# Kernel optimization log

Measured on AMD Instinct MI355X. Metric: run time of the kernel, lower is better.

The kernel has to match this reference:

```python
import jax, jax.numpy as jnp
import numpy as np

B, T, H = 16, 4096, 512


def setup_inputs() -> dict:
    key = jax.random.key(0)
    k1, k2, k3 = jax.random.split(key, 3)
    inputs = jax.random.normal(k1, (B, T, H), dtype=jnp.float32)
    # lengths in [1, T] so the global mean pool is well-defined
    lengths = jax.random.randint(k2, (B,), 1, T + 1, dtype=jnp.int32)
    mask = jax.random.randint(k3, (B, T), 0, 2).astype(bool)
    return {"inputs": inputs, "lengths": lengths, "mask": mask}


def _mean_pool(x, lengths):
    # length-masked mean pool: [B, T, H] -> [B, H]
    t = x.shape[1]
    valid = (jnp.arange(t)[None, :] < lengths[:, None]).astype(x.dtype)  # [B, T]
    summed = jnp.einsum('bth,bt->bh', x, valid)
    denom = jnp.maximum(lengths, 1).astype(x.dtype)[:, None]
    return summed / denom


def _span_select(x, mask):
    # Compact masked tokens to the front of each row (stable order), zero the tail.
    # Equivalent to the TF while_loop + scatter_nd/gather_nd compaction:
    # stable argsort of ~mask puts True positions first, in original order.
    order = jnp.argsort(jnp.logical_not(mask), axis=1, stable=True)  # [B, T]
    dense = jnp.take_along_axis(x, order[:, :, None], axis=1)        # [B, T, H]
    span_lengths = jnp.sum(mask.astype(jnp.int32), axis=1)           # [B]
    dense_mask = jnp.arange(x.shape[1])[None, :] < span_lengths[:, None]
    dense = dense * dense_mask[:, :, None].astype(x.dtype)
    return dense, span_lengths


def reference(inputs, lengths, mask):
    global_view = _mean_pool(inputs, lengths)            # [B, H]
    spans, span_lengths = _span_select(inputs, mask)     # [B, T, H], [B]
    local_view = _mean_pool(spans, span_lengths)         # [B, H]
    return jnp.concatenate([global_view, local_view], axis=-1)  # [B, 2H]
```

## Files before the change

### kernel.cpp

```cpp
#include <hip/hip_runtime.h>


constexpr int Bc = 16;
constexpr int Tc = 4096;
constexpr int Hc = 512;
constexpr int CHUNK  = 64;
constexpr int NCHUNK = Tc / CHUNK;
constexpr int NBLK   = Bc * NCHUNK;


__global__ __launch_bounds__(128) void glp_partial(
    const float* __restrict__ x,
    const int* __restrict__ lengths,
    const int* __restrict__ mask,
    float* __restrict__ pg,
    float* __restrict__ pl,
    int*   __restrict__ pcnt)
{
    const int blk  = blockIdx.x;
    const int b    = blk >> 6;
    const int c    = blk & (NCHUNK - 1);
    const int t0   = c * CHUNK;
    const int lane = threadIdx.x;
    const int len  = lengths[b];

    const float4* __restrict__ xb =
        (const float4*)x + ((size_t)b * Tc + t0) * (Hc / 4) + lane;
    const int* __restrict__ mb = mask + (size_t)b * Tc + t0;

    float4 g = make_float4(0.f, 0.f, 0.f, 0.f);
    float4 l = make_float4(0.f, 0.f, 0.f, 0.f);
    int mc = 0;

    for (int ii = 0; ii < CHUNK; ii += 8) {
        float4 v[8];
        int    m[8];
        #pragma unroll
        for (int j = 0; j < 8; ++j) {
            v[j] = xb[(size_t)(ii + j) * (Hc / 4)];
            m[j] = mb[ii + j];
        }
        #pragma unroll
        for (int j = 0; j < 8; ++j) {
            const float wg = (t0 + ii + j < len) ? 1.f : 0.f;
            const float wl = m[j] ? 1.f : 0.f;
            g.x = fmaf(v[j].x, wg, g.x); g.y = fmaf(v[j].y, wg, g.y);
            g.z = fmaf(v[j].z, wg, g.z); g.w = fmaf(v[j].w, wg, g.w);
            l.x = fmaf(v[j].x, wl, l.x); l.y = fmaf(v[j].y, wl, l.y);
            l.z = fmaf(v[j].z, wl, l.z); l.w = fmaf(v[j].w, wl, l.w);
            mc += (m[j] != 0);
        }
    }

    ((float4*)(pg + (size_t)blk * Hc))[lane] = g;
    ((float4*)(pl + (size_t)blk * Hc))[lane] = l;
    if (lane == 0) pcnt[blk] = mc;
}

__global__ __launch_bounds__(512) void glp_reduce(
    const float* __restrict__ pg,
    const float* __restrict__ pl,
    const int* __restrict__ pcnt,
    const int* __restrict__ lengths,
    float* __restrict__ out)
{
    const int b = blockIdx.x;
    const int h = threadIdx.x;
    const float* pgb = pg + (size_t)b * NCHUNK * Hc + h;
    const float* plb = pl + (size_t)b * NCHUNK * Hc + h;
    float gs = 0.f, ls = 0.f;
    #pragma unroll 8
    for (int c = 0; c < NCHUNK; ++c) {
        gs += pgb[(size_t)c * Hc];
        ls += plb[(size_t)c * Hc];
    }
    int cntv = 0;
    for (int c = 0; c < NCHUNK; ++c) cntv += pcnt[b * NCHUNK + c];
    out[b * 2 * Hc + h]      = gs / (float)max(lengths[b], 1);
    out[b * 2 * Hc + Hc + h] = ls / (float)max(cntv, 1);
}


__global__ __launch_bounds__(128) void glp_partial_atomic(
    const float* __restrict__ x,
    const int* __restrict__ lengths,
    const int* __restrict__ mask,
    float* __restrict__ gsum, float* __restrict__ lsum, int* __restrict__ cnt)
{
    const int blk  = blockIdx.x;
    const int b    = blk >> 6;
    const int c    = blk & (NCHUNK - 1);
    const int t0   = c * CHUNK;
    const int lane = threadIdx.x;
    const int len  = lengths[b];
    const float4* __restrict__ xb =
        (const float4*)x + ((size_t)b * Tc + t0) * (Hc / 4) + lane;
    const int* __restrict__ mb = mask + (size_t)b * Tc + t0;

    float4 g = make_float4(0.f, 0.f, 0.f, 0.f);
    float4 l = make_float4(0.f, 0.f, 0.f, 0.f);
    int mc = 0;
    for (int ii = 0; ii < CHUNK; ii += 8) {
        float4 v[8]; int m[8];
        #pragma unroll
        for (int j = 0; j < 8; ++j) { v[j] = xb[(size_t)(ii + j) * (Hc / 4)]; m[j] = mb[ii + j]; }
        #pragma unroll
        for (int j = 0; j < 8; ++j) {
            const float wg = (t0 + ii + j < len) ? 1.f : 0.f;
            const float wl = m[j] ? 1.f : 0.f;
            g.x = fmaf(v[j].x, wg, g.x); g.y = fmaf(v[j].y, wg, g.y);
            g.z = fmaf(v[j].z, wg, g.z); g.w = fmaf(v[j].w, wg, g.w);
            l.x = fmaf(v[j].x, wl, l.x); l.y = fmaf(v[j].y, wl, l.y);
            l.z = fmaf(v[j].z, wl, l.z); l.w = fmaf(v[j].w, wl, l.w);
            mc += (m[j] != 0);
        }
    }
    float* gp = gsum + b * Hc + lane * 4;
    float* lp = lsum + b * Hc + lane * 4;
    atomicAdd(gp + 0, g.x); atomicAdd(gp + 1, g.y);
    atomicAdd(gp + 2, g.z); atomicAdd(gp + 3, g.w);
    atomicAdd(lp + 0, l.x); atomicAdd(lp + 1, l.y);
    atomicAdd(lp + 2, l.z); atomicAdd(lp + 3, l.w);
    if (lane == 0) atomicAdd(cnt + b, mc);
}

__global__ __launch_bounds__(512) void glp_finalize(
    const float* __restrict__ gsum, const float* __restrict__ lsum,
    const int* __restrict__ cnt, const int* __restrict__ lengths,
    float* __restrict__ out)
{
    const int b = blockIdx.x;
    const int h = threadIdx.x;
    out[b * 2 * Hc + h]      = gsum[b * Hc + h] / (float)max(lengths[b], 1);
    out[b * 2 * Hc + Hc + h] = lsum[b * Hc + h] / (float)max(cnt[b], 1);
}

extern "C" void kernel_launch(void* const* d_in, const int* in_sizes, int n_in,
                              void* d_out, int out_size, void* d_ws, size_t ws_size,
                              hipStream_t stream) {
    const float* x     = (const float*)d_in[0];
    const int* lengths = (const int*)d_in[1];
    const int* mask    = (const int*)d_in[2];
    float* out = (float*)d_out;

    const size_t need = (size_t)NBLK * Hc * sizeof(float) * 2 + NBLK * sizeof(int);
    if (ws_size >= need) {
        float* pg  = (float*)d_ws;
        float* pl  = pg + (size_t)NBLK * Hc;
        int* pcnt  = (int*)(pl + (size_t)NBLK * Hc);
        glp_partial<<<NBLK, 128, 0, stream>>>(x, lengths, mask, pg, pl, pcnt);
        glp_reduce<<<Bc, Hc, 0, stream>>>(pg, pl, pcnt, lengths, out);
    } else {
        float* gsum = (float*)d_ws;
        float* lsum = gsum + Bc * Hc;
        int*   cnt  = (int*)(lsum + Bc * Hc);
        const size_t zb = (size_t)(2 * Bc * Hc) * sizeof(float) + Bc * sizeof(int);
        hipMemsetAsync(d_ws, 0, zb, stream);
        glp_partial_atomic<<<NBLK, 128, 0, stream>>>(x, lengths, mask, gsum, lsum, cnt);
        glp_finalize<<<Bc, Hc, 0, stream>>>(gsum, lsum, cnt, lengths, out);
    }
}
```

Baseline: 199.4 us.

## Split token chunks finer with two-way parallel rows and hierarchical reduce

Shrinks each partial-sum block to 16 tokens with 256 threads, two threads per column handling alternate tokens, and issues all loads up front. This raises the number of blocks and the loads in flight, to hide memory latency in the streaming pass. Because the partial buffer grows, a two-stage reduction replaces the single per-batch reduce. The cost is extra workspace traffic for the larger partial arrays.

```diff
diff --git a/kernel.cpp b/kernel.cpp
--- a/kernel.cpp
+++ b/kernel.cpp
@@ -4,12 +4,16 @@
 constexpr int Bc = 16;
 constexpr int Tc = 4096;
 constexpr int Hc = 512;
-constexpr int CHUNK  = 64;
-constexpr int NCHUNK = Tc / CHUNK;
-constexpr int NBLK   = Bc * NCHUNK;
-
-
-__global__ __launch_bounds__(128) void glp_partial(
+constexpr int H4 = Hc / 4;
+constexpr int CHUNK   = 16;
+constexpr int NCHUNK  = Tc / CHUNK;
+constexpr int NBLK    = Bc * NCHUNK;
+constexpr int NROW    = NBLK * 2;
+constexpr int ROWS_PB = NROW / Bc;
+constexpr int G2      = 8;
+constexpr int R2ROWS  = ROWS_PB / G2;
+
+__global__ __launch_bounds__(256) void glp_partial(
     const float* __restrict__ x,
     const int* __restrict__ lengths,
     const int* __restrict__ mask,
@@ -18,28 +22,128 @@
     int*   __restrict__ pcnt)
 {
     const int blk  = blockIdx.x;
-    const int b    = blk >> 6;
+    const int b    = blk >> 8;
     const int c    = blk & (NCHUNK - 1);
     const int t0   = c * CHUNK;
-    const int lane = threadIdx.x;
+    const int lane = threadIdx.x & 127;
+    const int par  = threadIdx.x >> 7;
     const int len  = lengths[b];
 
     const float4* __restrict__ xb =
-        (const float4*)x + ((size_t)b * Tc + t0) * (Hc / 4) + lane;
-    const int* __restrict__ mb = mask + (size_t)b * Tc + t0;
+        (const float4*)x + ((size_t)b * Tc + t0 + par) * H4 + lane;
+    const int* __restrict__ mb = mask + (size_t)b * Tc + t0 + par;
+
+    float4 v[8]; int m[8];
+    #pragma unroll
+    for (int j = 0; j < 8; ++j) {
+        v[j] = xb[(size_t)(2 * j) * H4];
+        m[j] = mb[2 * j];
+    }
 
     float4 g = make_float4(0.f, 0.f, 0.f, 0.f);
     float4 l = make_float4(0.f, 0.f, 0.f, 0.f);
     int mc = 0;
-
-    for (int ii = 0; ii < CHUNK; ii += 8) {
-        float4 v[8];
-        int    m[8];
+    #pragma unroll
+    for (int j = 0; j < 8; ++j) {
+        const float wg = (t0 + par + 2 * j < len) ? 1.f : 0.f;
+        const float wl = m[j] ? 1.f : 0.f;
+        g.x = fmaf(v[j].x, wg, g.x); g.y = fmaf(v[j].y, wg, g.y);
+        g.z = fmaf(v[j].z, wg, g.z); g.w = fmaf(v[j].w, wg, g.w);
+        l.x = fmaf(v[j].x, wl, l.x); l.y = fmaf(v[j].y, wl, l.y);
+        l.z = fmaf(v[j].z, wl, l.z); l.w = fmaf(v[j].w, wl, l.w);
+        mc += (m[j] != 0);
+    }
+
+    const int row = blk * 2 + par;
+    ((float4*)(pg + (size_t)row * Hc))[lane] = g;
+    ((float4*)(pl + (size_t)row * Hc))[lane] = l;
+    if (lane == 0) pcnt[row] = mc;
+}
+
+__global__ __launch_bounds__(128) void glp_reduce1(
+    const float* __restrict__ pg, const float* __restrict__ pl,
+    const int* __restrict__ pcnt,
+    float* __restrict__ qg, float* __restrict__ ql, int* __restrict__ qcnt)
+{
+    const int blk  = blockIdx.x;
+    const int r0   = blk * R2ROWS;
+    const int lane = threadIdx.x;
+    const float4* pg4 = (const float4*)pg + (size_t)r0 * H4 + lane;
+    const float4* pl4 = (const float4*)pl + (size_t)r0 * H4 + lane;
+
+    float4 gs = make_float4(0.f, 0.f, 0.f, 0.f);
+    float4 ls = make_float4(0.f, 0.f, 0.f, 0.f);
+    for (int r = 0; r < R2ROWS; r += 8) {
+        float4 a[8], d[8];
         #pragma unroll
         for (int j = 0; j < 8; ++j) {
-            v[j] = xb[(size_t)(ii + j) * (Hc / 4)];
-            m[j] = mb[ii + j];
+            a[j] = pg4[(size_t)(r + j) * H4];
+            d[j] = pl4[(size_t)(r + j) * H4];
         }
+        #pragma unroll
+        for (int j = 0; j < 8; ++j) {
+            gs.x += a[j].x; gs.y += a[j].y; gs.z += a[j].z; gs.w += a[j].w;
+            ls.x += d[j].x; ls.y += d[j].y; ls.z += d[j].z; ls.w += d[j].w;
+        }
+    }
+    ((float4*)(qg + (size_t)blk * Hc))[lane] = gs;
+    ((float4*)(ql + (size_t)blk * Hc))[lane] = ls;
+    if (lane == 0) {
+        int mc = 0;
+        for (int r = 0; r < R2ROWS; ++r) mc += pcnt[r0 + r];
+        qcnt[blk] = mc;
+    }
+}
+
+__global__ __launch_bounds__(128) void glp_reduce2(
+    const float* __restrict__ qg, const float* __restrict__ ql,
+    const int* __restrict__ qcnt, const int* __restrict__ lengths,
+    float* __restrict__ out)
+{
+    const int b    = blockIdx.x;
+    const int lane = threadIdx.x;
+    float4 gs = make_float4(0.f, 0.f, 0.f, 0.f);
+    float4 ls = make_float4(0.f, 0.f, 0.f, 0.f);
+    #pragma unroll
+    for (int k = 0; k < G2; ++k) {
+        float4 a = ((const float4*)(qg + (size_t)(b * G2 + k) * Hc))[lane];
+        float4 d = ((const float4*)(ql + (size_t)(b * G2 + k) * Hc))[lane];
+        gs.x += a.x; gs.y += a.y; gs.z += a.z; gs.w += a.w;
+        ls.x += d.x; ls.y += d.y; ls.z += d.z; ls.w += d.w;
+    }
+    int cnt = 0;
+    #pragma unroll
+    for (int k = 0; k < G2; ++k) cnt += qcnt[b * G2 + k];
+    const float invl = 1.f / (float)max(lengths[b], 1);
+    const float invc = 1.f / (float)max(cnt, 1);
+    gs.x *= invl; gs.y *= invl; gs.z *= invl; gs.w *= invl;
+    ls.x *= invc; ls.y *= invc; ls.z *= invc; ls.w *= invc;
+    ((float4*)(out + (size_t)b * 2 * Hc))[lane]      = gs;
+    ((float4*)(out + (size_t)b * 2 * Hc + Hc))[lane] = ls;
+}
+
+__global__ __launch_bounds__(128) void glp_partial_atomic(
+    const float* __restrict__ x, const int* __restrict__ lengths,
+    const int* __restrict__ mask,
+    float* __restrict__ gsum, float* __restrict__ lsum, int* __restrict__ cnt)
+{
+    const int blk  = blockIdx.x;
+    const int b    = blk >> 6;
+    const int c    = blk & 63;
+    const int t0   = c * 64;
+    const int lane = threadIdx.x;
+    const int len  = lengths[b];
+    const float4* __restrict__ xb =
+        (const float4*)x + ((size_t)b * Tc + t0) * H4 + lane;
+    const int* __restrict__ mb = mask + (size_t)b * Tc + t0;
+
+    float4 g = make_float4(0.f, 0.f, 0.f, 0.f);
+    float4 l = make_float4(0.f, 0.f, 0.f, 0.f);
+    int mc = 0;
+    for (int ii = 0; ii < 64; ii += 8) {
+        float4 v[8]; int m[8];
+        #pragma unroll
+        for (int j = 0; j < 8; ++j) { v[j] = xb[(size_t)(ii + j) * H4]; m[j] = mb[ii + j]; }
         #pragma unroll
         for (int j = 0; j < 8; ++j) {
             const float wg = (t0 + ii + j < len) ? 1.f : 0.f;
@@ -51,70 +155,6 @@
             mc += (m[j] != 0);
         }
     }
-
-    ((float4*)(pg + (size_t)blk * Hc))[lane] = g;
-    ((float4*)(pl + (size_t)blk * Hc))[lane] = l;
-    if (lane == 0) pcnt[blk] = mc;
-}
-
-__global__ __launch_bounds__(512) void glp_reduce(
-    const float* __restrict__ pg,
-    const float* __restrict__ pl,
-    const int* __restrict__ pcnt,
-    const int* __restrict__ lengths,
-    float* __restrict__ out)
-{
-    const int b = blockIdx.x;
-    const int h = threadIdx.x;
-    const float* pgb = pg + (size_t)b * NCHUNK * Hc + h;
-    const float* plb = pl + (size_t)b * NCHUNK * Hc + h;
-    float gs = 0.f, ls = 0.f;
-    #pragma unroll 8
-    for (int c = 0; c < NCHUNK; ++c) {
-        gs += pgb[(size_t)c * Hc];
-        ls += plb[(size_t)c * Hc];
-    }
-    int cntv = 0;
-    for (int c = 0; c < NCHUNK; ++c) cntv += pcnt[b * NCHUNK + c];
-    out[b * 2 * Hc + h]      = gs / (float)max(lengths[b], 1);
-    out[b * 2 * Hc + Hc + h] = ls / (float)max(cntv, 1);
-}
-
-
-__global__ __launch_bounds__(128) void glp_partial_atomic(
-    const float* __restrict__ x,
-    const int* __restrict__ lengths,
-    const int* __restrict__ mask,
-    float* __restrict__ gsum, float* __restrict__ lsum, int* __restrict__ cnt)
-{
-    const int blk  = blockIdx.x;
-    const int b    = blk >> 6;
-    const int c    = blk & (NCHUNK - 1);
-    const int t0   = c * CHUNK;
-    const int lane = threadIdx.x;
-    const int len  = lengths[b];
-    const float4* __restrict__ xb =
-        (const float4*)x + ((size_t)b * Tc + t0) * (Hc / 4) + lane;
-    const int* __restrict__ mb = mask + (size_t)b * Tc + t0;
-
-    float4 g = make_float4(0.f, 0.f, 0.f, 0.f);
-    float4 l = make_float4(0.f, 0.f, 0.f, 0.f);
-    int mc = 0;
-    for (int ii = 0; ii < CHUNK; ii += 8) {
-        float4 v[8]; int m[8];
-        #pragma unroll
-        for (int j = 0; j < 8; ++j) { v[j] = xb[(size_t)(ii + j) * (Hc / 4)]; m[j] = mb[ii + j]; }
-        #pragma unroll
-        for (int j = 0; j < 8; ++j) {
-            const float wg = (t0 + ii + j < len) ? 1.f : 0.f;
-            const float wl = m[j] ? 1.f : 0.f;
-            g.x = fmaf(v[j].x, wg, g.x); g.y = fmaf(v[j].y, wg, g.y);
-            g.z = fmaf(v[j].z, wg, g.z); g.w = fmaf(v[j].w, wg, g.w);
-            l.x = fmaf(v[j].x, wl, l.x); l.y = fmaf(v[j].y, wl, l.y);
-            l.z = fmaf(v[j].z, wl, l.z); l.w = fmaf(v[j].w, wl, l.w);
-            mc += (m[j] != 0);
-        }
-    }
     float* gp = gsum + b * Hc + lane * 4;
     float* lp = lsum + b * Hc + lane * 4;
     atomicAdd(gp + 0, g.x); atomicAdd(gp + 1, g.y);
@@ -143,20 +183,27 @@
     const int* mask    = (const int*)d_in[2];
     float* out = (float*)d_out;
 
-    const size_t need = (size_t)NBLK * Hc * sizeof(float) * 2 + NBLK * sizeof(int);
+    const size_t npg   = (size_t)NROW * Hc;
+    const size_t nq    = (size_t)Bc * G2 * Hc;
+    const size_t need  = (2 * npg + 2 * nq) * sizeof(float)
+                       + (NROW + Bc * G2) * sizeof(int);
     if (ws_size >= need) {
-        float* pg  = (float*)d_ws;
-        float* pl  = pg + (size_t)NBLK * Hc;
-        int* pcnt  = (int*)(pl + (size_t)NBLK * Hc);
-        glp_partial<<<NBLK, 128, 0, stream>>>(x, lengths, mask, pg, pl, pcnt);
-        glp_reduce<<<Bc, Hc, 0, stream>>>(pg, pl, pcnt, lengths, out);
+        float* pg   = (float*)d_ws;
+        float* pl   = pg + npg;
+        float* qg   = pl + npg;
+        float* ql   = qg + nq;
+        int*   pcnt = (int*)(ql + nq);
+        int*   qcnt = pcnt + NROW;
+        glp_partial<<<NBLK, 256, 0, stream>>>(x, lengths, mask, pg, pl, pcnt);
+        glp_reduce1<<<Bc * G2, 128, 0, stream>>>(pg, pl, pcnt, qg, ql, qcnt);
+        glp_reduce2<<<Bc, 128, 0, stream>>>(qg, ql, qcnt, lengths, out);
     } else {
         float* gsum = (float*)d_ws;
         float* lsum = gsum + Bc * Hc;
         int*   cnt  = (int*)(lsum + Bc * Hc);
         const size_t zb = (size_t)(2 * Bc * Hc) * sizeof(float) + Bc * sizeof(int);
         hipMemsetAsync(d_ws, 0, zb, stream);
-        glp_partial_atomic<<<NBLK, 128, 0, stream>>>(x, lengths, mask, gsum, lsum, cnt);
+        glp_partial_atomic<<<Bc * 64, 128, 0, stream>>>(x, lengths, mask, gsum, lsum, cnt);
         glp_finalize<<<Bc, Hc, 0, stream>>>(gsum, lsum, cnt, lengths, out);
     }
 }
```

After: 204.1 us. 2.3% more time.
